# Performance work log

Measured on AMD Instinct MI355X. Metric: run time of the kernel, lower is better.

The kernel has to match this reference:

```python
import jax, jax.numpy as jnp
import numpy as np

N_NODE = 100000
N_EDGE = 1600000
D_IN = 128
D_OUT = 128
D_EDGE = 32
EPS = 1e-10


def setup_inputs() -> dict:
    key = jax.random.key(0)
    ks = jax.random.split(key, 8)
    x = jax.random.normal(ks[0], (N_NODE, D_IN), dtype=jnp.float32)
    edge_list = jax.random.randint(ks[1], (N_EDGE, 2), 0, N_NODE, dtype=jnp.int32)
    edge_weights = jax.random.uniform(ks[2], (N_EDGE,), dtype=jnp.float32)
    edge_feature = jax.random.normal(ks[3], (N_EDGE, D_EDGE), dtype=jnp.float32)
    W_lin = jax.random.normal(ks[4], (D_OUT, D_IN), dtype=jnp.float32) * 0.05
    b_lin = jnp.zeros((D_OUT,), dtype=jnp.float32)
    W_edge = jax.random.normal(ks[5], (D_IN, D_EDGE), dtype=jnp.float32) * 0.05
    b_edge = jnp.zeros((D_IN,), dtype=jnp.float32)
    return {"x": x, "edge_list": edge_list, "edge_weights": edge_weights,
            "edge_feature": edge_feature, "W_lin": W_lin, "b_lin": b_lin,
            "W_edge": W_edge, "b_edge": b_edge}


def reference(x, edge_list, edge_weights, edge_feature, W_lin, b_lin, W_edge, b_edge):
    N = x.shape[0]
    src = edge_list[:, 0]  # node_in
    dst = edge_list[:, 1]  # node_out
    loops = jnp.arange(N, dtype=src.dtype)
    node_in = jnp.concatenate([src, loops])    # [E+N]
    node_out = jnp.concatenate([dst, loops])   # [E+N]
    ew = jnp.concatenate([edge_weights, jnp.ones((N,), x.dtype)])  # [E+N]
    # weighted degrees (torchdrug convention) + 1 for self loops
    deg_in = jax.ops.segment_sum(edge_weights, src, num_segments=N) + 1.0
    deg_out = jax.ops.segment_sum(edge_weights, dst, num_segments=N) + 1.0
    # symmetric degree normalization per (extended) edge
    w = ew / (jnp.sqrt(deg_in[node_in] * deg_out[node_out]) + EPS)  # [E+N]
    # sparse adj.T @ x: gather source features, scale, scatter-add to dest
    update = jax.ops.segment_sum(w[:, None] * x[node_in], node_out, num_segments=N)
    # edge-feature contribution (zeros for self loops)
    e = edge_feature @ W_edge.T + b_edge                        # [E, D_IN]
    e = jnp.concatenate([e, jnp.zeros((N, e.shape[1]), x.dtype)])
    update = update + jax.ops.segment_sum(w[:, None] * e, node_out, num_segments=N)
    # combine: linear + relu
    return jax.nn.relu(update @ W_lin.T + b_lin)
```

## Files before the change

### kernel.cpp

```cpp
#include <hip/hip_runtime.h>

#define N_NODES 100000
#define N_EDGES 1600000
#define D 128
#define DE 32
#define SCAN_CHUNK 1024
#define N_CHUNKS ((N_NODES + SCAN_CHUNK - 1) / SCAN_CHUNK)
#define POS_BLOCKS (N_EDGES / 2 / 256)
#define XH_BLOCKS (N_NODES * D / 8 / 256)

typedef int v4i __attribute__((ext_vector_type(4)));


__device__ inline float bflo(unsigned u) {
  return __uint_as_float(u << 16);
}
__device__ inline float bfhi(unsigned u) {
  return __uint_as_float(u & 0xFFFF0000u);
}
__device__ inline unsigned pk_bf2(float lo, float hi) {
  unsigned a = __float_as_uint(lo), b = __float_as_uint(hi);
  a = (a + 0x7FFFu + ((a >> 16) & 1)) >> 16;
  b = (b + 0x7FFFu + ((b >> 16) & 1)) >> 16;
  return a | (b << 16);
}

__global__ __launch_bounds__(256) void init_kernel(int* __restrict__ z) {
  int idx = blockIdx.x * 256 + threadIdx.x;
  if (idx < 5 * N_NODES) z[idx] = 0;
}

__global__ __launch_bounds__(256) void pre_kernel(
    const int4* __restrict__ el2, int* __restrict__ cursor,
    int2* __restrict__ pos2, const float4* __restrict__ x4,
    uint4* __restrict__ xh4) {
  int b = blockIdx.x;
  if (b < POS_BLOCKS) {
    int i = b * 256 + threadIdx.x;
    if (i >= N_EDGES / 2) return;
    int4 e = el2[i];
    int2 p;
    p.x = atomicAdd(&cursor[e.y], 1);
    p.y = atomicAdd(&cursor[e.w], 1);
    pos2[i] = p;
  } else {
    int i = (b - POS_BLOCKS) * 256 + threadIdx.x;
    if (i >= N_NODES * D / 8) return;
    float4 f0 = x4[2 * i], f1 = x4[2 * i + 1];
    uint4 o;
    o.x = pk_bf2(f0.x, f0.y);
    o.y = pk_bf2(f0.z, f0.w);
    o.z = pk_bf2(f1.x, f1.y);
    o.w = pk_bf2(f1.z, f1.w);
    xh4[i] = o;
  }
}

__global__ __launch_bounds__(256) void scan1_kernel(
    const int* __restrict__ counts, int* __restrict__ partial,
    int* __restrict__ blocksum) {
  __shared__ int lds[256];
  int t = threadIdx.x;
  int base = blockIdx.x * SCAN_CHUNK + t * 4;
  int c[4];
  int s = 0;
#pragma unroll
  for (int k = 0; k < 4; k++) {
    c[k] = (base + k < N_NODES) ? counts[base + k] : 0;
    s += c[k];
  }
  lds[t] = s;
  __syncthreads();
  for (int off = 1; off < 256; off <<= 1) {
    int tmp = (t >= off) ? lds[t - off] : 0;
    __syncthreads();
    lds[t] += tmp;
    __syncthreads();
  }
  int run = lds[t] - s;
#pragma unroll
  for (int k = 0; k < 4; k++) {
    int v = base + k;
    if (v < N_NODES) partial[v] = run;
    run += c[k];
  }
  if (t == 255) blocksum[blockIdx.x] = lds[255];
}

__global__ __launch_bounds__(128) void scan2_kernel(
    const int* __restrict__ blocksum, int* __restrict__ blockoff) {
  __shared__ int lds[128];
  int t = threadIdx.x;
  int v = (t < N_CHUNKS) ? blocksum[t] : 0;
  lds[t] = v;
  __syncthreads();
  for (int off = 1; off < 128; off <<= 1) {
    int tmp = (t >= off) ? lds[t - off] : 0;
    __syncthreads();
    lds[t] += tmp;
    __syncthreads();
  }
  if (t < N_CHUNKS) blockoff[t] = lds[t] - v;
}

__global__ __launch_bounds__(256) void place_kernel(
    const int4* __restrict__ el2, const float2* __restrict__ ew2,
    const int2* __restrict__ pos2, const int* __restrict__ partial,
    const int* __restrict__ blockoff, float* __restrict__ deg4,
    int4* __restrict__ rec) {
  int i = blockIdx.x * 256 + threadIdx.x;
  if (i >= N_EDGES / 2) return;
  int4 e = el2[i];
  float2 w = ew2[i];
  int2 p = pos2[i];
  int r0 = (threadIdx.x & 3) * N_NODES;
  atomicAdd(&deg4[r0 + e.x], w.x);
  atomicAdd(&deg4[r0 + e.z], w.y);
  int4 rA, rB;
  rA.x = e.x; rA.y = 2 * i;     rA.z = __float_as_int(w.x); rA.w = 0;
  rB.x = e.z; rB.y = 2 * i + 1; rB.z = __float_as_int(w.y); rB.w = 0;
  rec[partial[e.y] + blockoff[e.y >> 10] + p.x] = rA;
  rec[partial[e.w] + blockoff[e.w >> 10] + p.y] = rB;
}

__global__ __launch_bounds__(256) void rdi_kernel(
    const float* __restrict__ deg4, float* __restrict__ rdi) {
  int v = blockIdx.x * 256 + threadIdx.x;
  if (v >= N_NODES) return;
  rdi[v] = rsqrtf(1.f + deg4[v] + deg4[N_NODES + v] + deg4[2 * N_NODES + v] +
                  deg4[3 * N_NODES + v]);
}

__global__ __launch_bounds__(256) void wrec_kernel(
    int4* __restrict__ rec, const float* __restrict__ rdi) {
  int i = blockIdx.x * 256 + threadIdx.x;
  if (i >= N_EDGES) return;
  int4 r = rec[i];
  r.w = __float_as_int(__int_as_float(r.z) * rdi[r.x]);
  rec[i] = r;
}

template <bool XH16>
__global__ __launch_bounds__(256) void gather_fused_kernel(
    const float* __restrict__ x, const ushort* __restrict__ xh,
    const float* __restrict__ ef, const int* __restrict__ partial,
    const int* __restrict__ blockoff, const int* __restrict__ counts,
    const int4* __restrict__ rec, const float* __restrict__ rdi,
    const float* __restrict__ W_edge, const float* __restrict__ b_edge,
    float* __restrict__ out) {
  __shared__ __align__(16) float we[128 * 36];
  __shared__ float beS[128];
  int t = threadIdx.x;
#pragma unroll
  for (int i = 0; i < 4; ++i) {
    int f = t + i * 256;
    int r = f >> 3, kq = f & 7;
    *(float4*)&we[r * 36 + 4 * kq] = *(const float4*)&W_edge[r * DE + 4 * kq];
  }
  if (t < 128) beS[t] = b_edge[t];
  __syncthreads();

  int wid = t >> 6, lane = t & 63;
  int v = blockIdx.x * 4 + wid;
  if (v >= N_NODES) return;
  int start = partial[v] + blockoff[v >> 10];
  int cnt = counts[v];
  int lane31 = lane & 31;
  bool lowhalf = lane < 32;

  float A0 = 0.f, A1 = 0.f, B0 = 0.f, B1 = 0.f;
  float C0 = 0.f, C1 = 0.f, E0 = 0.f, E1 = 0.f;
  float ga = 0.f, gb = 0.f, gc = 0.f, gd = 0.f, dsum = 0.f, wsv = 0.f;

#define EFLOAD(eid) __builtin_nontemporal_load(&ef[(size_t)(eid)*DE + lane31])

  for (int base = 0; base < cnt; base += 64) {
    int nb = cnt - base;
    if (nb > 64) nb = 64;
    int s_l = 0, e_l = 0;
    float w_l = 0.f;
    if (lane < nb) {
      v4i rv = __builtin_nontemporal_load(
          (const v4i*)&rec[start + base + lane]);
      s_l = rv.x;
      e_l = rv.y;
      dsum += __int_as_float(rv.z);
      w_l = __int_as_float(rv.w);
      wsv += w_l;
    }
    int i = 0;
    for (; i + 8 <= nb; i += 8) {
      int s0 = __shfl(s_l, i + 0), s1 = __shfl(s_l, i + 1);
      int s2 = __shfl(s_l, i + 2), s3 = __shfl(s_l, i + 3);
      int s4 = __shfl(s_l, i + 4), s5 = __shfl(s_l, i + 5);
      int s6 = __shfl(s_l, i + 6), s7 = __shfl(s_l, i + 7);
      float w0 = __shfl(w_l, i + 0), w1 = __shfl(w_l, i + 1);
      float w2 = __shfl(w_l, i + 2), w3 = __shfl(w_l, i + 3);
      float w4 = __shfl(w_l, i + 4), w5 = __shfl(w_l, i + 5);
      float w6 = __shfl(w_l, i + 6), w7 = __shfl(w_l, i + 7);
      int hh = lane >> 5;
      int eA = __shfl(e_l, i + 0 + hh), eB = __shfl(e_l, i + 2 + hh);
      int eC = __shfl(e_l, i + 4 + hh), eD = __shfl(e_l, i + 6 + hh);
      float wA = lowhalf ? w0 : w1, wB = lowhalf ? w2 : w3;
      float wC = lowhalf ? w4 : w5, wD = lowhalf ? w6 : w7;
      ga = fmaf(wA, EFLOAD(eA), ga);
      gb = fmaf(wB, EFLOAD(eB), gb);
      gc = fmaf(wC, EFLOAD(eC), gc);
      gd = fmaf(wD, EFLOAD(eD), gd);
      if (XH16) {
        unsigned u0 = ((const unsigned*)(xh + (size_t)s0 * D))[lane];
        unsigned u1 = ((const unsigned*)(xh + (size_t)s1 * D))[lane];
        unsigned u2 = ((const unsigned*)(xh + (size_t)s2 * D))[lane];
        unsigned u3 = ((const unsigned*)(xh + (size_t)s3 * D))[lane];
        unsigned u4 = ((const unsigned*)(xh + (size_t)s4 * D))[lane];
        unsigned u5 = ((const unsigned*)(xh + (size_t)s5 * D))[lane];
        unsigned u6 = ((const unsigned*)(xh + (size_t)s6 * D))[lane];
        unsigned u7 = ((const unsigned*)(xh + (size_t)s7 * D))[lane];
        A0 = fmaf(w0, bflo(u0), A0); A1 = fmaf(w0, bfhi(u0), A1);
        B0 = fmaf(w1, bflo(u1), B0); B1 = fmaf(w1, bfhi(u1), B1);
        C0 = fmaf(w2, bflo(u2), C0); C1 = fmaf(w2, bfhi(u2), C1);
        E0 = fmaf(w3, bflo(u3), E0); E1 = fmaf(w3, bfhi(u3), E1);
        A0 = fmaf(w4, bflo(u4), A0); A1 = fmaf(w4, bfhi(u4), A1);
        B0 = fmaf(w5, bflo(u5), B0); B1 = fmaf(w5, bfhi(u5), B1);
        C0 = fmaf(w6, bflo(u6), C0); C1 = fmaf(w6, bfhi(u6), C1);
        E0 = fmaf(w7, bflo(u7), E0); E1 = fmaf(w7, bfhi(u7), E1);
      } else {
        float2 u0 = ((const float2*)(x + (size_t)s0 * D))[lane];
        float2 u1 = ((const float2*)(x + (size_t)s1 * D))[lane];
        float2 u2 = ((const float2*)(x + (size_t)s2 * D))[lane];
        float2 u3 = ((const float2*)(x + (size_t)s3 * D))[lane];
        float2 u4 = ((const float2*)(x + (size_t)s4 * D))[lane];
        float2 u5 = ((const float2*)(x + (size_t)s5 * D))[lane];
        float2 u6 = ((const float2*)(x + (size_t)s6 * D))[lane];
        float2 u7 = ((const float2*)(x + (size_t)s7 * D))[lane];
        A0 = fmaf(w0, u0.x, A0); A1 = fmaf(w0, u0.y, A1);
        B0 = fmaf(w1, u1.x, B0); B1 = fmaf(w1, u1.y, B1);
        C0 = fmaf(w2, u2.x, C0); C1 = fmaf(w2, u2.y, C1);
        E0 = fmaf(w3, u3.x, E0); E1 = fmaf(w3, u3.y, E1);
        A0 = fmaf(w4, u4.x, A0); A1 = fmaf(w4, u4.y, A1);
        B0 = fmaf(w5, u5.x, B0); B1 = fmaf(w5, u5.y, B1);
        C0 = fmaf(w6, u6.x, C0); C1 = fmaf(w6, u6.y, C1);
        E0 = fmaf(w7, u7.x, E0); E1 = fmaf(w7, u7.y, E1);
      }
    }
    for (; i + 2 <= nb; i += 2) {
      int s0 = __shfl(s_l, i), s1 = __shfl(s_l, i + 1);
      float w0 = __shfl(w_l, i), w1 = __shfl(w_l, i + 1);
      int eE = __shfl(e_l, i + (lane >> 5));
      float wE = lowhalf ? w0 : w1;
      ga = fmaf(wE, EFLOAD(eE), ga);
      if (XH16) {
        unsigned u0 = ((const unsigned*)(xh + (size_t)s0 * D))[lane];
        unsigned u1 = ((const unsigned*)(xh + (size_t)s1 * D))[lane];
        A0 = fmaf(w0, bflo(u0), A0); A1 = fmaf(w0, bfhi(u0), A1);
        B0 = fmaf(w1, bflo(u1), B0); B1 = fmaf(w1, bfhi(u1), B1);
      } else {
        float2 u0 = ((const float2*)(x + (size_t)s0 * D))[lane];
        float2 u1 = ((const float2*)(x + (size_t)s1 * D))[lane];
        A0 = fmaf(w0, u0.x, A0); A1 = fmaf(w0, u0.y, A1);
        B0 = fmaf(w1, u1.x, B0); B1 = fmaf(w1, u1.y, B1);
      }
    }
    if (i < nb) {
      int s0 = __shfl(s_l, i);
      float w0 = __shfl(w_l, i);
      int eA = __shfl(e_l, i);
      if (lowhalf) ga = fmaf(w0, EFLOAD(eA), ga);
      if (XH16) {
        unsigned u0 = ((const unsigned*)(xh + (size_t)s0 * D))[lane];
        A0 = fmaf(w0, bflo(u0), A0);
        A1 = fmaf(w0, bfhi(u0), A1);
      } else {
        float2 u0 = ((const float2*)(x + (size_t)s0 * D))[lane];
        A0 = fmaf(w0, u0.x, A0);
        A1 = fmaf(w0, u0.y, A1);
      }
    }
  }
#undef EFLOAD
  float a0 = (A0 + B0) + (C0 + E0);
  float a1 = (A1 + B1) + (C1 + E1);
#pragma unroll
  for (int off = 32; off; off >>= 1) {
    dsum += __shfl_xor(dsum, off);
    wsv += __shfl_xor(wsv, off);
  }
  float rdo = rsqrtf(1.f + dsum);
  float gk = (ga + gb) + (gc + gd);
  gk += __shfl(gk, (lane + 32) & 63);

  int half = lane >> 1;
  float v0 = __shfl(a0, half), v1 = __shfl(a1, half);
  float accLo = (lane & 1) ? v1 : v0;
  float q0 = __shfl(a0, 32 + half), q1 = __shfl(a1, 32 + half);
  float accHi = (lane & 1) ? q1 : q0;

  size_t ro = (size_t)v * D;
  float xs0, xs1;
  if (XH16) {
    xs0 = __uint_as_float((unsigned)xh[ro + lane] << 16);
    xs1 = __uint_as_float((unsigned)xh[ro + lane + 64] << 16);
  } else {
    xs0 = x[ro + lane];
    xs1 = x[ro + lane + 64];
  }
  float rdiv = rdi[v];
  float s0 = accLo + rdiv * xs0 + wsv * beS[lane];
  float s1 = accHi + rdiv * xs1 + wsv * beS[lane + 64];
#pragma unroll
  for (int kq = 0; kq < 8; ++kq) {
    float4 w0 = *(const float4*)&we[lane * 36 + 4 * kq];
    float4 w1 = *(const float4*)&we[(lane + 64) * 36 + 4 * kq];
    float g0 = __shfl(gk, 4 * kq);
    float g1 = __shfl(gk, 4 * kq + 1);
    float g2 = __shfl(gk, 4 * kq + 2);
    float g3 = __shfl(gk, 4 * kq + 3);
    s0 += g0 * w0.x + g1 * w0.y + g2 * w0.z + g3 * w0.w;
    s1 += g0 * w1.x + g1 * w1.y + g2 * w1.z + g3 * w1.w;
  }
  out[ro + lane] = rdo * s0;
  out[ro + lane + 64] = rdo * s1;
}

__global__ __launch_bounds__(256, 3) void gemm2_kernel(
    const float* __restrict__ W_lin, const float* __restrict__ b_lin,
    float* __restrict__ out) {
  __shared__ __align__(16) float xs[128 * 32];
  __shared__ __align__(16) float wl[128 * 32];
  int t = threadIdx.x;
  int tn = t & 15, tm = t >> 4;
  int m0 = 4 * tm, n0 = 4 * tn;
  int vbase = blockIdx.x * 128;
  float acc[8][8] = {};

  for (int ks = 0; ks < D; ks += 32) {
    __syncthreads();
#pragma unroll
    for (int i = 0; i < 4; ++i) {
      int f = t + i * 256;
      int r = f >> 3, kq = f & 7;
      int sw = (4 * kq) ^ (4 * ((r >> 2) & 7));
      float4 xv = make_float4(0.f, 0.f, 0.f, 0.f);
      if (vbase + r < N_NODES)
        xv = *(const float4*)&out[(size_t)(vbase + r) * D + ks + 4 * kq];
      *(float4*)&xs[r * 32 + sw] = xv;
      *(float4*)&wl[r * 32 + sw] = *(const float4*)&W_lin[r * D + ks + 4 * kq];
    }
    __syncthreads();
#pragma unroll 1
    for (int kq = 0; kq < 8; ++kq) {
      int sa = (4 * kq) ^ (4 * (tm & 7));
      int sb = (4 * kq) ^ (4 * (tn & 7));
      float4 a[8];
#pragma unroll
      for (int i = 0; i < 4; ++i) {
        a[i] = *(const float4*)&xs[(m0 + i) * 32 + sa];
        a[4 + i] = *(const float4*)&xs[(m0 + 64 + i) * 32 + sa];
      }
#pragma unroll
      for (int j = 0; j < 8; ++j) {
        int rj = (j < 4) ? (n0 + j) : (n0 + 60 + j);
        float4 b = *(const float4*)&wl[rj * 32 + sb];
#pragma unroll
        for (int i = 0; i < 8; ++i) {
          acc[i][j] += a[i].x * b.x + a[i].y * b.y + a[i].z * b.z +
                       a[i].w * b.w;
        }
      }
    }
  }

  float bl[8];
#pragma unroll
  for (int j = 0; j < 4; ++j) {
    bl[j] = b_lin[n0 + j];
    bl[4 + j] = b_lin[n0 + 64 + j];
  }
#pragma unroll
  for (int i = 0; i < 8; ++i) {
    int m = vbase + m0 + (i < 4 ? i : 64 + i - 4);
    if (m >= N_NODES) continue;
    float4 o0, o1;
    o0.x = fmaxf(acc[i][0] + bl[0], 0.f);
    o0.y = fmaxf(acc[i][1] + bl[1], 0.f);
    o0.z = fmaxf(acc[i][2] + bl[2], 0.f);
    o0.w = fmaxf(acc[i][3] + bl[3], 0.f);
    o1.x = fmaxf(acc[i][4] + bl[4], 0.f);
    o1.y = fmaxf(acc[i][5] + bl[5], 0.f);
    o1.z = fmaxf(acc[i][6] + bl[6], 0.f);
    o1.w = fmaxf(acc[i][7] + bl[7], 0.f);
    *(float4*)&out[(size_t)m * D + n0] = o0;
    *(float4*)&out[(size_t)m * D + n0 + 64] = o1;
  }
}

extern "C" void kernel_launch(void* const* d_in, const int* in_sizes, int n_in,
                              void* d_out, int out_size, void* d_ws,
                              size_t ws_size, hipStream_t stream) {
  const float* x      = (const float*)d_in[0];
  const int*   el     = (const int*)d_in[1];
  const float* ew     = (const float*)d_in[2];
  const float* ef     = (const float*)d_in[3];
  const float* W_lin  = (const float*)d_in[4];
  const float* b_lin  = (const float*)d_in[5];
  const float* W_edge = (const float*)d_in[6];
  const float* b_edge = (const float*)d_in[7];

  float* outp = (float*)d_out;

  char* base = (char*)d_ws;
  size_t off = 0;
  int4* rec      = (int4*)(base + off); off += (size_t)N_EDGES * 16;
  ushort* xh     = (ushort*)(base + off); off += (size_t)N_NODES * D * 2;
  int*  pos      = (int*)(base + off);  off += (size_t)N_EDGES * 4;
  float* deg4    = (float*)(base + off); off += (size_t)4 * N_NODES * 4;
  int*  cursor   = (int*)(base + off);  off += (size_t)N_NODES * 4;
  int*  partial  = (int*)(base + off);  off += (size_t)N_NODES * 4;
  int*  blocksum = (int*)(base + off);  off += 512;
  int*  blockoff = (int*)(base + off);  off += 512;
  float* rdi     = (float*)(base + off); off += (size_t)N_NODES * 4;
  const size_t REQ_FAST = off;
  bool fast = (ws_size >= REQ_FAST);
  if (!fast) {
    off = (size_t)N_EDGES * 16;
    pos      = (int*)(base + off);  off += (size_t)N_EDGES * 4;
    deg4     = (float*)(base + off); off += (size_t)4 * N_NODES * 4;
    cursor   = (int*)(base + off);  off += (size_t)N_NODES * 4;
    partial  = (int*)(base + off);  off += (size_t)N_NODES * 4;
    blocksum = (int*)(base + off);  off += 512;
    blockoff = (int*)(base + off);  off += 512;
    rdi      = (float*)(base + off); off += (size_t)N_NODES * 4;
    xh       = nullptr;
  }

  hipLaunchKernelGGL(init_kernel, dim3((5 * N_NODES + 255) / 256), dim3(256),
                     0, stream, (int*)deg4);
  hipLaunchKernelGGL(pre_kernel, dim3(fast ? POS_BLOCKS + XH_BLOCKS
                                           : POS_BLOCKS),
                     dim3(256), 0, stream, (const int4*)el, cursor, (int2*)pos,
                     (const float4*)x, (uint4*)xh);
  hipLaunchKernelGGL(scan1_kernel, dim3(N_CHUNKS), dim3(256), 0, stream,
                     cursor, partial, blocksum);
  hipLaunchKernelGGL(scan2_kernel, dim3(1), dim3(128), 0, stream, blocksum,
                     blockoff);
  hipLaunchKernelGGL(place_kernel, dim3((N_EDGES / 2 + 255) / 256), dim3(256),
                     0, stream, (const int4*)el, (const float2*)ew,
                     (const int2*)pos, partial, blockoff, deg4, rec);
  hipLaunchKernelGGL(rdi_kernel, dim3((N_NODES + 255) / 256), dim3(256), 0,
                     stream, deg4, rdi);
  hipLaunchKernelGGL(wrec_kernel, dim3((N_EDGES + 255) / 256), dim3(256), 0,
                     stream, rec, rdi);
  if (fast) {
    hipLaunchKernelGGL(gather_fused_kernel<true>, dim3((N_NODES + 3) / 4),
                       dim3(256), 0, stream, x, xh, ef, partial, blockoff,
                       cursor, rec, rdi, W_edge, b_edge, outp);
  } else {
    hipLaunchKernelGGL(gather_fused_kernel<false>, dim3((N_NODES + 3) / 4),
                       dim3(256), 0, stream, x, xh, ef, partial, blockoff,
                       cursor, rec, rdi, W_edge, b_edge, outp);
  }
  hipLaunchKernelGGL(gemm2_kernel, dim3((N_NODES + 127) / 128), dim3(256), 0,
                     stream, W_lin, b_lin, outp);
}
```

Before: 401.5 us.

## Use bf16 MFMA for final linear layer and fold edge-weight scaling into gather

Replaces the FP32 FMA tiled GEMM for the final linear+ReLU with a bf16 MFMA (16x16x32) kernel. The whole W_lin is converted to bf16 in shared memory and activation tiles are converted per K-step. It also removes the separate wrec pass that rewrote every edge record with its normalized weight, and instead computes w*rdi[src] inside the gather. This drops one full read and write of the 1.6M-entry record array and one launch. The costs are bf16 rounding in the final GEMM and one extra rdi lookup per edge in the gather.

```diff
diff --git a/kernel.cpp b/kernel.cpp
--- a/kernel.cpp
+++ b/kernel.cpp
@@ -10,6 +10,8 @@
 #define XH_BLOCKS (N_NODES * D / 8 / 256)
 
 typedef int v4i __attribute__((ext_vector_type(4)));
+typedef __attribute__((ext_vector_type(8))) short bf16x8;
+typedef __attribute__((ext_vector_type(4))) float f32x4;
 
 
 __device__ inline float bflo(unsigned u) {
@@ -131,15 +133,6 @@
                   deg4[3 * N_NODES + v]);
 }
 
-__global__ __launch_bounds__(256) void wrec_kernel(
-    int4* __restrict__ rec, const float* __restrict__ rdi) {
-  int i = blockIdx.x * 256 + threadIdx.x;
-  if (i >= N_EDGES) return;
-  int4 r = rec[i];
-  r.w = __float_as_int(__int_as_float(r.z) * rdi[r.x]);
-  rec[i] = r;
-}
-
 template <bool XH16>
 __global__ __launch_bounds__(256) void gather_fused_kernel(
     const float* __restrict__ x, const ushort* __restrict__ xh,
@@ -184,8 +177,9 @@
           (const v4i*)&rec[start + base + lane]);
       s_l = rv.x;
       e_l = rv.y;
-      dsum += __int_as_float(rv.z);
-      w_l = __int_as_float(rv.w);
+      float wraw = __int_as_float(rv.z);
+      w_l = wraw * rdi[s_l];
+      dsum += wraw;
       wsv += w_l;
     }
     int i = 0;
@@ -322,75 +316,75 @@
   out[ro + lane + 64] = rdo * s1;
 }
 
-__global__ __launch_bounds__(256, 3) void gemm2_kernel(
+__global__ __launch_bounds__(256) void gemm2_mfma_kernel(
     const float* __restrict__ W_lin, const float* __restrict__ b_lin,
     float* __restrict__ out) {
-  __shared__ __align__(16) float xs[128 * 32];
-  __shared__ __align__(16) float wl[128 * 32];
+  __shared__ __align__(16) ushort Asb[128 * 40];
+  __shared__ __align__(16) ushort Wsb[128 * 132];
   int t = threadIdx.x;
-  int tn = t & 15, tm = t >> 4;
-  int m0 = 4 * tm, n0 = 4 * tn;
   int vbase = blockIdx.x * 128;
-  float acc[8][8] = {};
-
-  for (int ks = 0; ks < D; ks += 32) {
+
+#pragma unroll
+  for (int i = 0; i < 16; ++i) {
+    int idx = t + i * 256;
+    int r = idx >> 5;
+    int c = (idx & 31) * 4;
+    float4 f = *(const float4*)&W_lin[r * D + c];
+    uint2 u;
+    u.x = pk_bf2(f.x, f.y);
+    u.y = pk_bf2(f.z, f.w);
+    *(uint2*)&Wsb[r * 132 + c] = u;
+  }
+
+  int lane = t & 63, w = t >> 6;
+  int l15 = lane & 15, kg = lane >> 4;
+  f32x4 acc[2][8] = {};
+
+  for (int ks = 0; ks < 4; ++ks) {
     __syncthreads();
 #pragma unroll
     for (int i = 0; i < 4; ++i) {
-      int f = t + i * 256;
-      int r = f >> 3, kq = f & 7;
-      int sw = (4 * kq) ^ (4 * ((r >> 2) & 7));
-      float4 xv = make_float4(0.f, 0.f, 0.f, 0.f);
+      int idx = t + i * 256;
+      int r = idx >> 3;
+      int c = (idx & 7) * 4;
+      float4 f = make_float4(0.f, 0.f, 0.f, 0.f);
       if (vbase + r < N_NODES)
-        xv = *(const float4*)&out[(size_t)(vbase + r) * D + ks + 4 * kq];
-      *(float4*)&xs[r * 32 + sw] = xv;
-      *(float4*)&wl[r * 32 + sw] = *(const float4*)&W_lin[r * D + ks + 4 * kq];
-    }
-    __syncthreads();
-#pragma unroll 1
-    for (int kq = 0; kq < 8; ++kq) {
-      int sa = (4 * kq) ^ (4 * (tm & 7));
-      int sb = (4 * kq) ^ (4 * (tn & 7));
-      float4 a[8];
-#pragma unroll
-      for (int i = 0; i < 4; ++i) {
-        a[i] = *(const float4*)&xs[(m0 + i) * 32 + sa];
-        a[4 + i] = *(const float4*)&xs[(m0 + 64 + i) * 32 + sa];
+        f = *(const float4*)&out[(size_t)(vbase + r) * D + ks * 32 + c];
+      uint2 u;
+      u.x = pk_bf2(f.x, f.y);
+      u.y = pk_bf2(f.z, f.w);
+      *(uint2*)&Asb[r * 40 + c] = u;
+    }
+    __syncthreads();
+    bf16x8 a0 = *(const bf16x8*)&Asb[(w * 32 + l15) * 40 + kg * 8];
+    bf16x8 a1 = *(const bf16x8*)&Asb[(w * 32 + 16 + l15) * 40 + kg * 8];
+#pragma unroll
+    for (int nt = 0; nt < 8; ++nt) {
+      const ushort* bp = &Wsb[(nt * 16 + l15) * 132 + ks * 32 + kg * 8];
+      uint2 q0 = *(const uint2*)bp;
+      uint2 q1 = *(const uint2*)(bp + 4);
+      uint4 bu = make_uint4(q0.x, q0.y, q1.x, q1.y);
+      bf16x8 bf = *(bf16x8*)&bu;
+      acc[0][nt] =
+          __builtin_amdgcn_mfma_f32_16x16x32_bf16(a0, bf, acc[0][nt], 0, 0, 0);
+      acc[1][nt] =
+          __builtin_amdgcn_mfma_f32_16x16x32_bf16(a1, bf, acc[1][nt], 0, 0, 0);
+    }
+  }
+
+#pragma unroll
+  for (int nt = 0; nt < 8; ++nt) {
+    int col = nt * 16 + l15;
+    float bl = b_lin[col];
+#pragma unroll
+    for (int mt = 0; mt < 2; ++mt) {
+#pragma unroll
+      for (int j = 0; j < 4; ++j) {
+        int row = vbase + w * 32 + mt * 16 + kg * 4 + j;
+        if (row < N_NODES)
+          out[(size_t)row * D + col] = fmaxf(acc[mt][nt][j] + bl, 0.f);
       }
-#pragma unroll
-      for (int j = 0; j < 8; ++j) {
-        int rj = (j < 4) ? (n0 + j) : (n0 + 60 + j);
-        float4 b = *(const float4*)&wl[rj * 32 + sb];
-#pragma unroll
-        for (int i = 0; i < 8; ++i) {
-          acc[i][j] += a[i].x * b.x + a[i].y * b.y + a[i].z * b.z +
-                       a[i].w * b.w;
-        }
-      }
-    }
-  }
-
-  float bl[8];
-#pragma unroll
-  for (int j = 0; j < 4; ++j) {
-    bl[j] = b_lin[n0 + j];
-    bl[4 + j] = b_lin[n0 + 64 + j];
-  }
-#pragma unroll
-  for (int i = 0; i < 8; ++i) {
-    int m = vbase + m0 + (i < 4 ? i : 64 + i - 4);
-    if (m >= N_NODES) continue;
-    float4 o0, o1;
-    o0.x = fmaxf(acc[i][0] + bl[0], 0.f);
-    o0.y = fmaxf(acc[i][1] + bl[1], 0.f);
-    o0.z = fmaxf(acc[i][2] + bl[2], 0.f);
-    o0.w = fmaxf(acc[i][3] + bl[3], 0.f);
-    o1.x = fmaxf(acc[i][4] + bl[4], 0.f);
-    o1.y = fmaxf(acc[i][5] + bl[5], 0.f);
-    o1.z = fmaxf(acc[i][6] + bl[6], 0.f);
-    o1.w = fmaxf(acc[i][7] + bl[7], 0.f);
-    *(float4*)&out[(size_t)m * D + n0] = o0;
-    *(float4*)&out[(size_t)m * D + n0 + 64] = o1;
+    }
   }
 }
 
@@ -448,8 +442,6 @@
                      (const int2*)pos, partial, blockoff, deg4, rec);
   hipLaunchKernelGGL(rdi_kernel, dim3((N_NODES + 255) / 256), dim3(256), 0,
                      stream, deg4, rdi);
-  hipLaunchKernelGGL(wrec_kernel, dim3((N_EDGES + 255) / 256), dim3(256), 0,
-                     stream, rec, rdi);
   if (fast) {
     hipLaunchKernelGGL(gather_fused_kernel<true>, dim3((N_NODES + 3) / 4),
                        dim3(256), 0, stream, x, xh, ef, partial, blockoff,
@@ -459,6 +451,6 @@
                        dim3(256), 0, stream, x, xh, ef, partial, blockoff,
                        cursor, rec, rdi, W_edge, b_edge, outp);
   }
-  hipLaunchKernelGGL(gemm2_kernel, dim3((N_NODES + 127) / 128), dim3(256), 0,
-                     stream, W_lin, b_lin, outp);
-}
+  hipLaunchKernelGGL(gemm2_mfma_kernel, dim3((N_NODES + 127) / 128), dim3(256),
+                     0, stream, W_lin, b_lin, outp);
+}
```

After: 356.1 us. 11.3% less time.
